# Kernel tuning notes

Hardware: AMD Instinct MI355X
Metric: run time of the kernel (lower is better)

Reference implementation:

```python
import jax, jax.numpy as jnp
import numpy as np

B, T, E, H = 8, 1024, 1024, 16
D = E // H  # head_dim = 64
MAX_OFFSET = 0.5


def setup_inputs() -> dict:
    key = jax.random.key(0)
    ks = jax.random.split(key, 12)
    s = 0.02
    return {
        "query": jax.random.normal(ks[0], (B, T, E), jnp.float32),
        "key_": jax.random.normal(ks[1], (B, T, E), jnp.float32),
        "value": jax.random.normal(ks[2], (B, T, E), jnp.float32),
        "Wq": jax.random.normal(ks[3], (E, E), jnp.float32) * s,
        "bq": jnp.zeros((E,), jnp.float32),
        "Wk": jax.random.normal(ks[4], (E, E), jnp.float32) * s,
        "bk": jnp.zeros((E,), jnp.float32),
        "Wv": jax.random.normal(ks[5], (E, E), jnp.float32) * s,
        "bv": jnp.zeros((E,), jnp.float32),
        "Wo": jax.random.normal(ks[6], (E, E), jnp.float32) * s,
        "bo": jnp.zeros((E,), jnp.float32),
        "bias_table": jax.random.normal(ks[7], (2 * T - 1, H), jnp.float32) * s,
        "offset": jax.random.normal(ks[8], (1,), jnp.float32) * 0.1,
    }


def _temporal_bias(bias_table, offset):
    # relative position index: [T, T] in [0, 2T-2]
    coords = jnp.arange(T)
    rel = (coords[:, None] - coords[None, :]) + (T - 1)
    bounded = jnp.tanh(offset) * MAX_OFFSET  # scalar (shape (1,))
    adj = jnp.clip(rel.astype(jnp.float32) + bounded, 0.0, 2.0 * T - 2.0)
    lo = jnp.floor(adj).astype(jnp.int32)
    hi = jnp.ceil(adj).astype(jnp.int32)
    w = adj - lo.astype(jnp.float32)  # [T, T]
    lo_val = bias_table[lo]  # [T, T, H]
    hi_val = bias_table[hi]  # [T, T, H]
    bias = lo_val * (1.0 - w[..., None]) + hi_val * w[..., None]
    # -> [1, H, T, T]
    return jnp.transpose(bias, (2, 0, 1))[None]


def reference(query, key_, value, Wq, bq, Wk, bk, Wv, bv, Wo, bo, bias_table, offset):
    scale = D ** -0.5
    # torch Linear: x @ W.T + b
    q = (jnp.einsum('bte,fe->btf', query, Wq) + bq).reshape(B, T, H, D).transpose(0, 2, 1, 3)
    k = (jnp.einsum('bte,fe->btf', key_, Wk) + bk).reshape(B, T, H, D).transpose(0, 2, 1, 3)
    v = (jnp.einsum('bte,fe->btf', value, Wv) + bv).reshape(B, T, H, D).transpose(0, 2, 1, 3)
    scores = jnp.einsum('bhqd,bhkd->bhqk', q, k) * scale  # [B, H, T, T]
    scores = scores + _temporal_bias(bias_table, offset)
    attn = jax.nn.softmax(scores, axis=-1)
    out = jnp.einsum('bhqk,bhkd->bhqd', attn, v)  # [B, H, T, D]
    out = out.transpose(0, 2, 1, 3).reshape(B, T, E)
    return jnp.einsum('bte,fe->btf', out, Wo) + bo
```

## Files before the change

kernel.cpp:

```cpp
#include <hip/hip_runtime.h>
#include <hip/hip_bf16.h>
#include <stdint.h>

#define B_ 8
#define T_ 1024
#define E_ 1024
#define H_ 16
#define D_ 64
#define NREL 2047

using bf16 = __hip_bfloat16;
typedef __attribute__((ext_vector_type(8))) short bhalf8;
typedef __attribute__((ext_vector_type(4))) float f32x4;

typedef __attribute__((address_space(3))) uint32_t lds32_t;
typedef const __attribute__((address_space(1))) uint32_t glb32_t;
__device__ __forceinline__ void gld_lds16(const bf16* g, bf16* l) {
  __builtin_amdgcn_global_load_lds((glb32_t*)(const void*)g, (lds32_t*)(void*)l, 16, 0, 0);
}

__global__ __launch_bounds__(256) void cvt_f32_bf16(const float* __restrict__ s,
                                                    bf16* __restrict__ d, int n) {
  const int i = (blockIdx.x * 256 + threadIdx.x) * 8;
  if (i >= n) return;
  const float4 a = *(const float4*)(s + i);
  const float4 b = *(const float4*)(s + i + 4);
  bf16 t[8];
  t[0] = __float2bfloat16(a.x); t[1] = __float2bfloat16(a.y);
  t[2] = __float2bfloat16(a.z); t[3] = __float2bfloat16(a.w);
  t[4] = __float2bfloat16(b.x); t[5] = __float2bfloat16(b.y);
  t[6] = __float2bfloat16(b.z); t[7] = __float2bfloat16(b.w);
  *(bhalf8*)(d + i) = *(const bhalf8*)t;
}

__global__ void bias_pre(const float* __restrict__ table, const float* __restrict__ offset,
                         float* __restrict__ db) {
  const int idx = blockIdx.x * 256 + threadIdx.x;
  if (idx >= NREL * H_) return;
  const int r = idx >> 4;
  const int h = idx & 15;
  const float bounded = tanhf(offset[0]) * 0.5f;
  float adj = (float)r + bounded;
  adj = fminf(fmaxf(adj, 0.f), 2046.f);
  const int lo = (int)floorf(adj);
  const int hi = (int)ceilf(adj);
  const float wgt = adj - (float)lo;
  const float v = table[lo * H_ + h] * (1.f - wgt) + table[hi * H_ + h] * wgt;
  db[h * NREL + r] = v;
}

template <int SCATTER, int F32OUT>
__global__ __launch_bounds__(256) void gemm_bt(const bf16* __restrict__ A,
                                               const bf16* __restrict__ W,
                                               const float* __restrict__ bias,
                                               void* __restrict__ dst_) {
  __shared__ bf16 As[128 * 32];
  __shared__ bf16 Bs[128 * 32];
  const int tid = threadIdx.x;
  const int lane = tid & 63;
  const int w = tid >> 6;
  const int quad = lane >> 4;
  const int l15 = lane & 15;
  const int m0 = blockIdx.x * 128;
  const int n0 = blockIdx.y * 128;
  const int wm = (w >> 1) * 64;
  const int wn = (w & 1) * 64;

  const f32x4 zero4 = {0.f, 0.f, 0.f, 0.f};
  f32x4 acc[4][4];
#pragma unroll
  for (int i = 0; i < 4; ++i)
#pragma unroll
    for (int j = 0; j < 4; ++j) acc[i][j] = zero4;

  const int srow0 = w * 32 + (lane >> 2);
  const int scol = (lane & 3) * 8;
  const bf16* Ag = A + (size_t)(m0 + srow0) * E_ + scol;
  const bf16* Wg = W + (size_t)(n0 + srow0) * E_ + scol;
  bf16* As0 = As + w * 1024 + lane * 8;
  bf16* Bs0 = Bs + w * 1024 + lane * 8;

  for (int kt = 0; kt < 32; ++kt) {
    __syncthreads();
    const int kc = kt * 32;
    gld_lds16(Ag + kc, As0);
    gld_lds16(Ag + (size_t)16 * E_ + kc, As0 + 512);
    gld_lds16(Wg + kc, Bs0);
    gld_lds16(Wg + (size_t)16 * E_ + kc, Bs0 + 512);
    __syncthreads();

    bhalf8 af[4], bfr[4];
#pragma unroll
    for (int t = 0; t < 4; ++t) {
      af[t] = *(const bhalf8*)(As + (wm + t * 16 + l15) * 32 + quad * 8);
      bfr[t] = *(const bhalf8*)(Bs + (wn + t * 16 + l15) * 32 + quad * 8);
    }
#pragma unroll
    for (int mt = 0; mt < 4; ++mt)
#pragma unroll
      for (int nt = 0; nt < 4; ++nt)
        acc[mt][nt] = __builtin_amdgcn_mfma_f32_16x16x32_bf16(af[mt], bfr[nt], acc[mt][nt], 0, 0, 0);
  }

#pragma unroll
  for (int mt = 0; mt < 4; ++mt) {
#pragma unroll
    for (int nt = 0; nt < 4; ++nt) {
      const int n = n0 + wn + nt * 16 + l15;
      const float bv = bias[n];
#pragma unroll
      for (int r = 0; r < 4; ++r) {
        const int m = m0 + wm + mt * 16 + quad * 4 + r;
        const float v = acc[mt][nt][r] + bv;
        if (SCATTER) {
          const int bb = m >> 10, t = m & 1023, hh = n >> 6, d = n & 63;
          ((bf16*)dst_)[(((size_t)bb * H_ + hh) * T_ + t) * D_ + d] = __float2bfloat16(v);
        } else if (F32OUT) {
          ((float*)dst_)[(size_t)m * E_ + n] = v;
        } else {
          ((bf16*)dst_)[(size_t)m * E_ + n] = __float2bfloat16(v);
        }
      }
    }
  }
}

__global__ __launch_bounds__(256, 4) void attn_kernel(const bf16* __restrict__ Q,
                                                      const bf16* __restrict__ K,
                                                      const bf16* __restrict__ V,
                                                      const float* __restrict__ db,
                                                      bf16* __restrict__ xout) {
  const int tid = threadIdx.x;
  const int lane = tid & 63;
  const int w = tid >> 6;
  const int quad = lane >> 4;
  const int l15 = lane & 15;
  const int bh = blockIdx.x;
  const int h = bh & 15;
  const int b = bh >> 4;
  const int q0 = blockIdx.y * 128;

  __shared__ bf16 Vt[64][72];
  __shared__ bf16 Ps[4][32][80];
  __shared__ float dbs[1152];

  const size_t base = (size_t)bh * T_ * D_;
  const bf16* Qp = Q + base;
  const bf16* Kp = K + base;
  const bf16* Vp = V + base;
  const float* dbh = db + h * NREL;

  for (int t = tid; t < 1151; t += 256) dbs[t] = dbh[q0 + t];

  const int qw = q0 + w * 32;
  bhalf8 aq[2][2];
#pragma unroll
  for (int mt = 0; mt < 2; ++mt)
#pragma unroll
    for (int ks = 0; ks < 2; ++ks)
      aq[mt][ks] = *(const bhalf8*)(Qp + (size_t)(qw + mt * 16 + l15) * D_ + ks * 32 + quad * 8);

  const f32x4 zero4 = {0.f, 0.f, 0.f, 0.f};
  f32x4 o[2][4];
#pragma unroll
  for (int mt = 0; mt < 2; ++mt)
#pragma unroll
    for (int nt = 0; nt < 4; ++nt) o[mt][nt] = zero4;
  float mrow[2] = {-1e30f, -1e30f};
  float lrow[2] = {0.f, 0.f};

  for (int it = 0; it < 16; ++it) {
    const int kb = it * 64;
    __syncthreads();
#pragma unroll
    for (int s = 0; s < 2; ++s) {
      const int idx = tid + s * 256;
      const int row = idx >> 3;
      const int c8 = (idx & 7) * 8;
      bhalf8 vv = *(const bhalf8*)(Vp + (size_t)(kb + row) * D_ + c8);
      const bf16* vp = (const bf16*)&vv;
      const int kvp = (row + c8) & 63;
#pragma unroll
      for (int j = 0; j < 8; ++j) Vt[c8 + j][kvp] = vp[j];
    }
    __syncthreads();

    f32x4 s4[2][4];
    __builtin_amdgcn_s_setprio(1);
#pragma unroll
    for (int nt = 0; nt < 4; ++nt) {
      const bf16* kr = Kp + (size_t)(kb + nt * 16 + l15) * D_ + quad * 8;
      const bhalf8 bk0 = *(const bhalf8*)kr;
      const bhalf8 bk1 = *(const bhalf8*)(kr + 32);
#pragma unroll
      for (int mt = 0; mt < 2; ++mt) {
        f32x4 a = zero4;
        a = __builtin_amdgcn_mfma_f32_16x16x32_bf16(bk0, aq[mt][0], a, 0, 0, 0);
        a = __builtin_amdgcn_mfma_f32_16x16x32_bf16(bk1, aq[mt][1], a, 0, 0, 0);
        s4[mt][nt] = a;
      }
    }
    __builtin_amdgcn_s_setprio(0);

#pragma unroll
    for (int mt = 0; mt < 2; ++mt) {
      const int ib = w * 32 + mt * 16 + l15 + 1023 - kb;
      float tmx = -1e30f;
#pragma unroll
      for (int nt = 0; nt < 4; ++nt) {
#pragma unroll
        for (int r = 0; r < 4; ++r) {
          const float sv = s4[mt][nt][r] * 0.125f + dbs[ib - nt * 16 - quad * 4 - r];
          s4[mt][nt][r] = sv;
          tmx = fmaxf(tmx, sv);
        }
      }
      tmx = fmaxf(tmx, __shfl_xor(tmx, 16, 64));
      tmx = fmaxf(tmx, __shfl_xor(tmx, 32, 64));
      if (!__all(tmx - mrow[mt] <= 8.0f)) {
        const float mnew = fmaxf(mrow[mt], tmx);
        const float alpha = __expf(mrow[mt] - mnew);
        mrow[mt] = mnew;
        lrow[mt] *= alpha;
#pragma unroll
        for (int nt = 0; nt < 4; ++nt) o[mt][nt] *= alpha;
      }
      const float mcur = mrow[mt];
      float sum = 0.f;
#pragma unroll
      for (int nt = 0; nt < 4; ++nt) {
#pragma unroll
        for (int r = 0; r < 4; ++r) {
          const float p = __expf(s4[mt][nt][r] - mcur);
          s4[mt][nt][r] = p;
          sum += p;
        }
      }
      sum += __shfl_xor(sum, 16, 64);
      sum += __shfl_xor(sum, 32, 64);
      lrow[mt] += sum;

#pragma unroll
      for (int nt = 0; nt < 4; ++nt) {
        alignas(8) bf16 t4[4];
#pragma unroll
        for (int r = 0; r < 4; ++r) t4[r] = __float2bfloat16(s4[mt][nt][r]);
        *(uint2*)&Ps[w][mt * 16 + l15][nt * 16 + quad * 4] = *(const uint2*)t4;
      }
    }

    bhalf8 pb[2][2];
#pragma unroll
    for (int mt = 0; mt < 2; ++mt)
#pragma unroll
      for (int ks = 0; ks < 2; ++ks)
        pb[mt][ks] = *(const bhalf8*)&Ps[w][mt * 16 + l15][ks * 32 + quad * 8];
    const int rot = (l15 >> 3);
    __builtin_amdgcn_s_setprio(1);
#pragma unroll
    for (int nt = 0; nt < 4; ++nt) {
      const int drow = nt * 16 + l15;
#pragma unroll
      for (int ks = 0; ks < 2; ++ks) {
        const int gp = (4 * ks + quad + 2 * nt + rot) & 7;
        const bhalf8 vb = *(const bhalf8*)&Vt[drow][gp * 8];
#pragma unroll
        for (int mt = 0; mt < 2; ++mt)
          o[mt][nt] = __builtin_amdgcn_mfma_f32_16x16x32_bf16(vb, pb[mt][ks], o[mt][nt], 0, 0, 0);
      }
    }
    __builtin_amdgcn_s_setprio(0);
  }

#pragma unroll
  for (int mt = 0; mt < 2; ++mt) {
    const float inv = 1.f / lrow[mt];
    const int q = qw + mt * 16 + l15;
#pragma unroll
    for (int nt = 0; nt < 4; ++nt) {
      alignas(8) bf16 t4[4];
#pragma unroll
      for (int r = 0; r < 4; ++r) t4[r] = __float2bfloat16(o[mt][nt][r] * inv);
      *(uint2*)&xout[((size_t)b * T_ + q) * E_ + h * D_ + nt * 16 + quad * 4] = *(const uint2*)t4;
    }
  }
}

extern "C" void kernel_launch(void* const* d_in, const int* in_sizes, int n_in,
                              void* d_out, int out_size, void* d_ws, size_t ws_size,
                              hipStream_t stream) {
  const float* query = (const float*)d_in[0];
  const float* key_  = (const float*)d_in[1];
  const float* value = (const float*)d_in[2];
  const float* Wq = (const float*)d_in[3];
  const float* bq = (const float*)d_in[4];
  const float* Wk = (const float*)d_in[5];
  const float* bk = (const float*)d_in[6];
  const float* Wv = (const float*)d_in[7];
  const float* bv = (const float*)d_in[8];
  const float* Wo = (const float*)d_in[9];
  const float* bo = (const float*)d_in[10];
  const float* table = (const float*)d_in[11];
  const float* offset = (const float*)d_in[12];
  float* out = (float*)d_out;

  char* ws = (char*)d_ws;
  const size_t ME = (size_t)B_ * T_ * E_;
  const size_t EE = (size_t)E_ * E_;
  float* db = (float*)ws;
  bf16* xc  = (bf16*)(ws + 131072);
  bf16* wc  = xc + ME;
  bf16* qb  = wc + 4 * EE;
  bf16* kb  = qb + ME;
  bf16* vb2 = kb + ME;
  bf16* x2  = vb2 + ME;

  dim3 bb(256, 1, 1);
  dim3 gg(64, 8, 1);
  const int gME = (int)(ME / 8 / 256);
  const int gEE = (int)(EE / 8 / 256);

  bias_pre<<<dim3(128), bb, 0, stream>>>(table, offset, db);

  cvt_f32_bf16<<<dim3(gEE), bb, 0, stream>>>(Wq, wc + 0 * EE, (int)EE);
  cvt_f32_bf16<<<dim3(gEE), bb, 0, stream>>>(Wk, wc + 1 * EE, (int)EE);
  cvt_f32_bf16<<<dim3(gEE), bb, 0, stream>>>(Wv, wc + 2 * EE, (int)EE);
  cvt_f32_bf16<<<dim3(gEE), bb, 0, stream>>>(Wo, wc + 3 * EE, (int)EE);

  cvt_f32_bf16<<<dim3(gME), bb, 0, stream>>>(query, xc, (int)ME);
  gemm_bt<1, 0><<<gg, bb, 0, stream>>>(xc, wc + 0 * EE, bq, qb);
  cvt_f32_bf16<<<dim3(gME), bb, 0, stream>>>(key_, xc, (int)ME);
  gemm_bt<1, 0><<<gg, bb, 0, stream>>>(xc, wc + 1 * EE, bk, kb);
  cvt_f32_bf16<<<dim3(gME), bb, 0, stream>>>(value, xc, (int)ME);
  gemm_bt<1, 0><<<gg, bb, 0, stream>>>(xc, wc + 2 * EE, bv, vb2);

  attn_kernel<<<dim3(128, 8, 1), bb, 0, stream>>>(qb, kb, vb2, db, x2);

  gemm_bt<0, 1><<<gg, bb, 0, stream>>>(x2, wc + 3 * EE, bo, out);
}
```

Measured before the change: 381.8 us.

## Prefetch K/V tiles into registers, use exp2 softmax, XOR-swizzle P buffer

The attention kernel now loads the next V tile into registers right after the barrier and issues the K fragment loads before the V transpose, so global latency overlaps compute. The bias table and score scale are pre-multiplied by log2(e) so the softmax can use the native exp2 instruction. The rescale threshold rises to 11 in log2 units to match the old threshold of 8. The P staging buffer uses an XOR swizzle instead of padding, and the output is staged through LDS so it can be written back in 16-byte coalesced stores. Register pressure rises from the prefetch buffers, which may hurt occupancy at launch bound 4.

Result: faster. 363.0 us (-4.9%).

```diff
diff --git a/kernel.cpp b/kernel.cpp
--- a/kernel.cpp
+++ b/kernel.cpp
@@ -46,7 +46,7 @@
   const int hi = (int)ceilf(adj);
   const float wgt = adj - (float)lo;
   const float v = table[lo * H_ + h] * (1.f - wgt) + table[hi * H_ + h] * wgt;
-  db[h * NREL + r] = v;
+  db[h * NREL + r] = v * 1.4426950408889634f;
 }
 
 template <int SCATTER, int F32OUT>
@@ -125,6 +125,10 @@
   }
 }
 
+__device__ __forceinline__ int ps_off(int row, int colbyte) {
+  return row * 128 + (colbyte ^ ((row & 7) << 4));
+}
+
 __global__ __launch_bounds__(256, 4) void attn_kernel(const bf16* __restrict__ Q,
                                                       const bf16* __restrict__ K,
                                                       const bf16* __restrict__ V,
@@ -141,7 +145,7 @@
   const int q0 = blockIdx.y * 128;
 
   __shared__ bf16 Vt[64][72];
-  __shared__ bf16 Ps[4][32][80];
+  __shared__ __align__(16) bf16 Ps[4][32 * 64];
   __shared__ float dbs[1152];
 
   const size_t base = (size_t)bh * T_ * D_;
@@ -169,34 +173,49 @@
   float mrow[2] = {-1e30f, -1e30f};
   float lrow[2] = {0.f, 0.f};
 
+  const int vrow0 = tid >> 3;
+  const int vc8 = (tid & 7) * 8;
+  bhalf8 vreg[2];
+  vreg[0] = *(const bhalf8*)(Vp + (size_t)vrow0 * D_ + vc8);
+  vreg[1] = *(const bhalf8*)(Vp + (size_t)(vrow0 + 32) * D_ + vc8);
+
+  char* const psw = (char*)&Ps[w][0];
+
   for (int it = 0; it < 16; ++it) {
     const int kb = it * 64;
+    bhalf8 bk[4][2];
+#pragma unroll
+    for (int nt = 0; nt < 4; ++nt) {
+      const bf16* kr = Kp + (size_t)(kb + nt * 16 + l15) * D_ + quad * 8;
+      bk[nt][0] = *(const bhalf8*)kr;
+      bk[nt][1] = *(const bhalf8*)(kr + 32);
+    }
+
     __syncthreads();
 #pragma unroll
     for (int s = 0; s < 2; ++s) {
-      const int idx = tid + s * 256;
-      const int row = idx >> 3;
-      const int c8 = (idx & 7) * 8;
-      bhalf8 vv = *(const bhalf8*)(Vp + (size_t)(kb + row) * D_ + c8);
-      const bf16* vp = (const bf16*)&vv;
-      const int kvp = (row + c8) & 63;
-#pragma unroll
-      for (int j = 0; j < 8; ++j) Vt[c8 + j][kvp] = vp[j];
+      const int row = vrow0 + s * 32;
+      const bf16* vp = (const bf16*)&vreg[s];
+      const int kvp = (row + vc8) & 63;
+#pragma unroll
+      for (int j = 0; j < 8; ++j) Vt[vc8 + j][kvp] = vp[j];
     }
     __syncthreads();
+    if (it < 15) {
+      const int kb2 = kb + 64;
+      vreg[0] = *(const bhalf8*)(Vp + (size_t)(kb2 + vrow0) * D_ + vc8);
+      vreg[1] = *(const bhalf8*)(Vp + (size_t)(kb2 + vrow0 + 32) * D_ + vc8);
+    }
 
     f32x4 s4[2][4];
     __builtin_amdgcn_s_setprio(1);
 #pragma unroll
     for (int nt = 0; nt < 4; ++nt) {
-      const bf16* kr = Kp + (size_t)(kb + nt * 16 + l15) * D_ + quad * 8;
-      const bhalf8 bk0 = *(const bhalf8*)kr;
-      const bhalf8 bk1 = *(const bhalf8*)(kr + 32);
 #pragma unroll
       for (int mt = 0; mt < 2; ++mt) {
         f32x4 a = zero4;
-        a = __builtin_amdgcn_mfma_f32_16x16x32_bf16(bk0, aq[mt][0], a, 0, 0, 0);
-        a = __builtin_amdgcn_mfma_f32_16x16x32_bf16(bk1, aq[mt][1], a, 0, 0, 0);
+        a = __builtin_amdgcn_mfma_f32_16x16x32_bf16(bk[nt][0], aq[mt][0], a, 0, 0, 0);
+        a = __builtin_amdgcn_mfma_f32_16x16x32_bf16(bk[nt][1], aq[mt][1], a, 0, 0, 0);
         s4[mt][nt] = a;
       }
     }
@@ -205,37 +224,41 @@
 #pragma unroll
     for (int mt = 0; mt < 2; ++mt) {
       const int ib = w * 32 + mt * 16 + l15 + 1023 - kb;
-      float tmx = -1e30f;
+      float mnt[4];
 #pragma unroll
       for (int nt = 0; nt < 4; ++nt) {
 #pragma unroll
         for (int r = 0; r < 4; ++r) {
-          const float sv = s4[mt][nt][r] * 0.125f + dbs[ib - nt * 16 - quad * 4 - r];
+          const float sv = s4[mt][nt][r] * 0.18033688011112042f + dbs[ib - nt * 16 - quad * 4 - r];
           s4[mt][nt][r] = sv;
-          tmx = fmaxf(tmx, sv);
         }
-      }
+        mnt[nt] = fmaxf(fmaxf(s4[mt][nt][0], s4[mt][nt][1]),
+                        fmaxf(s4[mt][nt][2], s4[mt][nt][3]));
+      }
+      float tmx = fmaxf(fmaxf(mnt[0], mnt[1]), fmaxf(mnt[2], mnt[3]));
       tmx = fmaxf(tmx, __shfl_xor(tmx, 16, 64));
       tmx = fmaxf(tmx, __shfl_xor(tmx, 32, 64));
-      if (!__all(tmx - mrow[mt] <= 8.0f)) {
+      if (!__all(tmx - mrow[mt] <= 11.0f)) {
         const float mnew = fmaxf(mrow[mt], tmx);
-        const float alpha = __expf(mrow[mt] - mnew);
+        const float alpha = __builtin_amdgcn_exp2f(mrow[mt] - mnew);
         mrow[mt] = mnew;
         lrow[mt] *= alpha;
 #pragma unroll
         for (int nt = 0; nt < 4; ++nt) o[mt][nt] *= alpha;
       }
       const float mcur = mrow[mt];
-      float sum = 0.f;
+      float psum[4];
 #pragma unroll
       for (int nt = 0; nt < 4; ++nt) {
-#pragma unroll
-        for (int r = 0; r < 4; ++r) {
-          const float p = __expf(s4[mt][nt][r] - mcur);
-          s4[mt][nt][r] = p;
-          sum += p;
-        }
-      }
+        float p0 = __builtin_amdgcn_exp2f(s4[mt][nt][0] - mcur);
+        float p1 = __builtin_amdgcn_exp2f(s4[mt][nt][1] - mcur);
+        float p2 = __builtin_amdgcn_exp2f(s4[mt][nt][2] - mcur);
+        float p3 = __builtin_amdgcn_exp2f(s4[mt][nt][3] - mcur);
+        s4[mt][nt][0] = p0; s4[mt][nt][1] = p1;
+        s4[mt][nt][2] = p2; s4[mt][nt][3] = p3;
+        psum[nt] = (p0 + p1) + (p2 + p3);
+      }
+      float sum = (psum[0] + psum[1]) + (psum[2] + psum[3]);
       sum += __shfl_xor(sum, 16, 64);
       sum += __shfl_xor(sum, 32, 64);
       lrow[mt] += sum;
@@ -245,7 +268,7 @@
         alignas(8) bf16 t4[4];
 #pragma unroll
         for (int r = 0; r < 4; ++r) t4[r] = __float2bfloat16(s4[mt][nt][r]);
-        *(uint2*)&Ps[w][mt * 16 + l15][nt * 16 + quad * 4] = *(const uint2*)t4;
+        *(uint2*)(psw + ps_off(mt * 16 + l15, nt * 32 + quad * 8)) = *(const uint2*)t4;
       }
     }
 
@@ -254,7 +277,7 @@
     for (int mt = 0; mt < 2; ++mt)
 #pragma unroll
       for (int ks = 0; ks < 2; ++ks)
-        pb[mt][ks] = *(const bhalf8*)&Ps[w][mt * 16 + l15][ks * 32 + quad * 8];
+        pb[mt][ks] = *(const bhalf8*)(psw + ps_off(mt * 16 + l15, ks * 64 + quad * 16));
     const int rot = (l15 >> 3);
     __builtin_amdgcn_s_setprio(1);
 #pragma unroll
@@ -275,14 +298,21 @@
 #pragma unroll
   for (int mt = 0; mt < 2; ++mt) {
     const float inv = 1.f / lrow[mt];
-    const int q = qw + mt * 16 + l15;
 #pragma unroll
     for (int nt = 0; nt < 4; ++nt) {
       alignas(8) bf16 t4[4];
 #pragma unroll
       for (int r = 0; r < 4; ++r) t4[r] = __float2bfloat16(o[mt][nt][r] * inv);
-      *(uint2*)&xout[((size_t)b * T_ + q) * E_ + h * D_ + nt * 16 + quad * 4] = *(const uint2*)t4;
-    }
+      *(uint2*)(psw + ps_off(mt * 16 + l15, nt * 32 + quad * 8)) = *(const uint2*)t4;
+    }
+  }
+#pragma unroll
+  for (int t = 0; t < 4; ++t) {
+    const int idx = t * 64 + lane;
+    const int row = idx >> 3;
+    const int c = idx & 7;
+    const bhalf8 val = *(const bhalf8*)(psw + ps_off(row, c * 16));
+    *(bhalf8*)&xout[((size_t)b * T_ + qw + row) * E_ + h * D_ + c * 8] = val;
   }
 }
 
```
